# Optimization experiments

Measured on AMD Instinct MI355X. Metric: run time of the kernel, lower is better.

Reference implementation:

```python
import jax, jax.numpy as jnp
import numpy as np
from itertools import product

D = 96  # input grid resolution; after subdivision it is 2*D = 192
N_VOX = 20000
C_IN = 64
C_OUT = 64

OFFSETS = jnp.array(list(product([-1, 0, 1], repeat=3)), dtype=jnp.int32)   # [27,3] conv neighborhood
CHILD = jnp.array(list(product([0, 1], repeat=3)), dtype=jnp.int32)        # [8,3] subdivision children


def _lin(coords, d):
    # linearize (z,y,x)-style coords into a flat index for the dense lookup grid
    return (coords[:, 0] * d + coords[:, 1]) * d + coords[:, 2]


def _submanifold_conv3d(coords, feats, W, b, d):
    """Submanifold sparse 3x3x3 conv: output only at active sites.
    coords: [N,3] int32, feats: [N,Cin], W: [27,Cin,Cout], b: [Cout]."""
    n = coords.shape[0]
    grid = jnp.full((d * d * d,), -1, dtype=jnp.int32).at[_lin(coords, d)].set(
        jnp.arange(n, dtype=jnp.int32))
    out = jnp.broadcast_to(b, (n, b.shape[0])).astype(feats.dtype)
    for k in range(27):  # fixed small kernel loop (unrolled under jit)
        nb = coords + OFFSETS[k]
        inb = jnp.all((nb >= 0) & (nb < d), axis=1)
        idx = grid[_lin(jnp.clip(nb, 0, d - 1), d)]
        mask = (inb & (idx >= 0)).astype(feats.dtype)
        f = feats[jnp.maximum(idx, 0)] * mask[:, None]  # gather active neighbors
        out = out + f @ W[k]
    return out


def setup_inputs() -> dict:
    rng = np.random.default_rng(0)
    lin = rng.choice(D ** 3, size=N_VOX, replace=False)  # unique active voxels
    coords = np.stack([lin // (D * D), (lin // D) % D, lin % D], axis=1).astype(np.int32)
    key = jax.random.key(0)
    k1, k2, k3, k4, k5 = jax.random.split(key, 5)
    scale = 1.0 / np.sqrt(27.0 * C_IN)
    return {
        "coords": jnp.asarray(coords),
        "feats": jax.random.normal(k1, (N_VOX, C_IN), jnp.float32),
        "W1": jax.random.normal(k2, (27, C_IN, C_OUT), jnp.float32) * scale,
        "b1": jax.random.normal(k3, (C_OUT,), jnp.float32) * 0.01,
        "W2": jax.random.normal(k4, (27, C_OUT, C_OUT), jnp.float32) * scale,
        "b2": jax.random.normal(k5, (C_OUT,), jnp.float32) * 0.01,
    }


def reference(coords, feats, W1, b1, W2, b2):
    # act_layers: SparseConv3d + SiLU
    h = jax.nn.silu(_submanifold_conv3d(coords, feats, W1, b1, D))
    n = coords.shape[0]
    coords2 = ((coords * 2)[:, None, :] + CHILD[None, :, :]).reshape(8 * n, 3)
    h2 = jnp.repeat(h, 8, axis=0)  # matches (N,8,C)->(8N,C) child order
    # out_layers: SparseConv3d + SiLU at doubled resolution
    return jax.nn.silu(_submanifold_conv3d(coords2, h2, W2, b2, 2 * D))
```

## Files before the change

kernel.cpp:

```cpp
#include <hip/hip_runtime.h>

#define D1 96
#define GRID_VOX (D1 * D1 * D1)
#define CAP1 32
#define CAP2S 8
#define OS 68

typedef __attribute__((ext_vector_type(8))) short short8_t;
typedef __attribute__((ext_vector_type(4))) float f32x4;

__device__ __forceinline__ unsigned short bf16rne(float x) {
    unsigned u = __float_as_uint(x);
    return (unsigned short)((u + 0x7FFF + ((u >> 16) & 1)) >> 16);
}
__device__ __forceinline__ void split2(float v, unsigned short& hi,
                                       unsigned short& lo) {
    hi = bf16rne(v);
    float hf = __uint_as_float((unsigned)hi << 16);
    lo = bf16rne(v - hf);
}
__device__ __forceinline__ float silu(float v) {
    return v / (1.f + __expf(-v));
}

__global__ void setup_kernel(const float* __restrict__ W1,
                             const float* __restrict__ W2,
                             int4* __restrict__ grid16,
                             unsigned short* __restrict__ Wpk1h,
                             unsigned short* __restrict__ Wpk1l,
                             unsigned short* __restrict__ Wpk2h,
                             unsigned short* __restrict__ Wpk2l,
                             float* __restrict__ W2e) {
    int b = blockIdx.x;
    if (b < 432) {
        grid16[b * 256 + threadIdx.x] = make_int4(0, 0, 0, 0);
        return;
    }
    int t = (b - 432) * 256 + threadIdx.x;
    if (t < 512) {
        int fid = t >> 6, l = t & 63;
        int kb = fid >> 2, c = fid & 3;
#pragma unroll
        for (int e = 0; e < 8; ++e) {
            int ci = kb * 32 + ((l >> 4) << 3) + e;
            int co = c * 16 + (l & 15);
            unsigned short hi, lo;
            split2(W1[13 * 4096 + ci * 64 + co], hi, lo);
            Wpk1h[(size_t)t * 8 + e] = hi;
            Wpk1l[(size_t)t * 8 + e] = lo;
        }
    } else if (t < 512 + 4096) {
        int u = t - 512;
        int fid = u >> 6, l = u & 63;
        int s = fid >> 3, kb = (fid >> 2) & 1, c = fid & 3;
        int s0 = (s >> 2) & 1, s1 = (s >> 1) & 1, s2 = s & 1;
#pragma unroll
        for (int e = 0; e < 8; ++e) {
            int ci = kb * 32 + ((l >> 4) << 3) + e;
            int co = c * 16 + (l & 15);
            float sum = 0.f;
            for (int o0 = -s0; o0 <= 1 - s0; ++o0)
                for (int o1 = -s1; o1 <= 1 - s1; ++o1)
                    for (int o2 = -s2; o2 <= 1 - s2; ++o2) {
                        int k = (o0 + 1) * 9 + (o1 + 1) * 3 + (o2 + 1);
                        sum += W2[k * 4096 + ci * 64 + co];
                    }
            unsigned short hi, lo;
            split2(sum, hi, lo);
            Wpk2h[(size_t)u * 8 + e] = hi;
            Wpk2l[(size_t)u * 8 + e] = lo;
        }
    } else {
        int r = t - 4608;
        if (r >= 64 * 4096) return;
        int sd = r >> 12, e = r & 4095;
        int s = sd >> 3, d = sd & 7;
        int sa[3] = { (s >> 2) & 1, (s >> 1) & 1, s & 1 };
        int da[3] = { (d >> 2) & 1, (d >> 1) & 1, d & 1 };
        int lo_[3], hi_[3];
        for (int a = 0; a < 3; ++a) {
            int p = sa[a] - 1 + da[a];
            int l = 2 * p - sa[a];     if (l < -1) l = -1;
            int h = 2 * p + 1 - sa[a]; if (h > 1) h = 1;
            lo_[a] = l; hi_[a] = h;
        }
        float sum = 0.f;
        for (int o0 = lo_[0]; o0 <= hi_[0]; ++o0)
            for (int o1 = lo_[1]; o1 <= hi_[1]; ++o1)
                for (int o2 = lo_[2]; o2 <= hi_[2]; ++o2) {
                    int k = (o0 + 1) * 9 + (o1 + 1) * 3 + (o2 + 1);
                    sum += W2[k * 4096 + e];
                }
        W2e[(size_t)sd * 4096 + e] = sum;
    }
}

__global__ void scatter_grid_kernel(const int* __restrict__ coords,
                                    unsigned short* __restrict__ grid, int n) {
    int i = blockIdx.x * blockDim.x + threadIdx.x;
    if (i < n)
        grid[(coords[3 * i] * D1 + coords[3 * i + 1]) * D1 + coords[3 * i + 2]] =
            (unsigned short)(i + 1);
}

__global__ void build_pairs_kernel(const int* __restrict__ coords,
                                   const unsigned short* __restrict__ grid,
                                   int* __restrict__ c1, int* __restrict__ p1,
                                   int* __restrict__ c2s, int* __restrict__ p2s,
                                   int n) {
    int i = blockIdx.x * blockDim.x + threadIdx.x;
    if (i >= n) return;
    int c0 = coords[3 * i], cc1 = coords[3 * i + 1], cc2 = coords[3 * i + 2];

    int jv[27];
#pragma unroll
    for (int k = 0; k < 27; ++k) {
        int o0 = k / 9 - 1, o1 = (k / 3) % 3 - 1, o2 = k % 3 - 1;
        int x0 = c0 + o0, x1 = cc1 + o1, x2 = cc2 + o2;
        bool inb = (unsigned)x0 < D1 && (unsigned)x1 < D1 && (unsigned)x2 < D1;
        jv[k] = inb ? (int)grid[(x0 * D1 + x1) * D1 + x2] - 1 : -1;
    }

    int n1 = 0;
    int n2[8] = {0, 0, 0, 0, 0, 0, 0, 0};
#pragma unroll
    for (int k = 0; k < 27; ++k) {
        if (k == 13) continue;
        int j = jv[k];
        if (j < 0) continue;
        int o0 = k / 9 - 1, o1 = (k / 3) % 3 - 1, o2 = k % 3 - 1;
        p1[(size_t)i * CAP1 + n1] = j | (k << 17);
        ++n1;
#pragma unroll
        for (int s = 0; s < 8; ++s) {
            int d0 = o0 + 1 - ((s >> 2) & 1);
            int d1 = o1 + 1 - ((s >> 1) & 1);
            int d2 = o2 + 1 - (s & 1);
            if (((d0 | d1 | d2) & ~1) == 0) {
                int d = (d0 << 2) | (d1 << 1) | d2;
                p2s[((size_t)i * 8 + s) * CAP2S + n2[s]] = j | (d << 17);
                ++n2[s];
            }
        }
    }
    c1[i] = n1;
#pragma unroll
    for (int s = 0; s < 8; ++s) c2s[i * 8 + s] = n2[s];
}

__device__ __forceinline__ void load_split_A(const float* __restrict__ src,
                                             int arow, int lane, short8_t& ah0,
                                             short8_t& al0, short8_t& ah1,
                                             short8_t& al1) {
    const float* ap = src + (size_t)arow * 64 + ((lane >> 4) << 3);
    f32x4 a0 = *(const f32x4*)(ap);
    f32x4 a1 = *(const f32x4*)(ap + 4);
    f32x4 a2 = *(const f32x4*)(ap + 32);
    f32x4 a3 = *(const f32x4*)(ap + 36);
#pragma unroll
    for (int e = 0; e < 4; ++e) {
        unsigned short hh, ll;
        split2(a0[e], hh, ll); ah0[e] = (short)hh; al0[e] = (short)ll;
        split2(a1[e], hh, ll); ah0[4 + e] = (short)hh; al0[4 + e] = (short)ll;
        split2(a2[e], hh, ll); ah1[e] = (short)hh; al1[e] = (short)ll;
        split2(a3[e], hh, ll); ah1[4 + e] = (short)hh; al1[4 + e] = (short)ll;
    }
}

__device__ __forceinline__ void dense_mfma8(const short8_t ah0, const short8_t al0,
                                            const short8_t ah1, const short8_t al1,
                                            const short8_t* __restrict__ Bh,
                                            const short8_t* __restrict__ Bl,
                                            const float* __restrict__ bias,
                                            float* __restrict__ oT, int w,
                                            int lane) {
    int c0 = (w >> 2) * 2;
#pragma unroll
    for (int cc = 0; cc < 2; ++cc) {
        int c = c0 + cc;
        short8_t bh0 = Bh[c * 64 + lane];
        short8_t bl0 = Bl[c * 64 + lane];
        short8_t bh1 = Bh[(4 + c) * 64 + lane];
        short8_t bl1 = Bl[(4 + c) * 64 + lane];
        f32x4 acc = {0.f, 0.f, 0.f, 0.f};
        acc = __builtin_amdgcn_mfma_f32_16x16x32_bf16(ah0, bh0, acc, 0, 0, 0);
        acc = __builtin_amdgcn_mfma_f32_16x16x32_bf16(al0, bh0, acc, 0, 0, 0);
        acc = __builtin_amdgcn_mfma_f32_16x16x32_bf16(ah0, bl0, acc, 0, 0, 0);
        acc = __builtin_amdgcn_mfma_f32_16x16x32_bf16(ah1, bh1, acc, 0, 0, 0);
        acc = __builtin_amdgcn_mfma_f32_16x16x32_bf16(al1, bh1, acc, 0, 0, 0);
        acc = __builtin_amdgcn_mfma_f32_16x16x32_bf16(ah1, bl1, acc, 0, 0, 0);
        int col = c * 16 + (lane & 15);
        float bb = bias[col];
#pragma unroll
        for (int r = 0; r < 4; ++r) {
            int row = (w & 3) * 16 + ((lane >> 4) << 2) + r;
            oT[row * OS + col] = acc[r] + bb;
        }
    }
}

__device__ __forceinline__ void scan64(int cnt, int lane, int* pfxs, int* cnts,
                                       int* nps) {
    int val = cnt;
#pragma unroll
    for (int off = 1; off < 64; off <<= 1) {
        int v2 = __shfl_up(val, off);
        if (lane >= off) val += v2;
    }
    pfxs[lane] = val - cnt;
    cnts[lane] = cnt;
    if (lane == 63) nps[0] = val;
}

__device__ __forceinline__ void fixup_loop(const float* __restrict__ src,
                                           const float* __restrict__ Wbase,
                                           const int* __restrict__ pl, int np,
                                           float fsc[8][2][64],
                                           float* __restrict__ oT, int w,
                                           int lane) {
    int it = 0;
#pragma unroll 1
    for (int p = w; p < np; p += 8, ++it) {
        int e = pl[p];
        int j = e & 0x1FFFF, tag = (e >> 17) & 31, row = (e >> 23) & 63;
        float fv = src[(size_t)j * 64 + lane];
        int buf = it & 1;
        fsc[w][buf][lane] = fv;
        const float* wk = Wbase + (size_t)tag * 4096;
        float a0 = 0.f, a1 = 0.f, a2 = 0.f, a3 = 0.f;
#pragma unroll
        for (int c4 = 0; c4 < 16; ++c4) {
            f32x4 fb = *(f32x4*)&fsc[w][buf][c4 * 4];
            a0 += fb[0] * wk[(c4 * 4 + 0) * 64 + lane];
            a1 += fb[1] * wk[(c4 * 4 + 1) * 64 + lane];
            a2 += fb[2] * wk[(c4 * 4 + 2) * 64 + lane];
            a3 += fb[3] * wk[(c4 * 4 + 3) * 64 + lane];
        }
        atomicAdd(&oT[row * OS + lane], (a0 + a1) + (a2 + a3));
    }
}

__global__ __launch_bounds__(512) void conv1_fused_kernel(
    const float* __restrict__ feats, const float* __restrict__ W1,
    const unsigned short* __restrict__ Wpk1h,
    const unsigned short* __restrict__ Wpk1l, const float* __restrict__ b1,
    const int* __restrict__ c1, const int* __restrict__ p1,
    float* __restrict__ h, int n) {
    __shared__ __align__(16) float oT[64 * OS];
    __shared__ __align__(16) float fsc[8][2][64];
    __shared__ int pl[1664];
    __shared__ int pfxs[64], cnts_s[64], nps[1];
    int base = blockIdx.x * 64;
    int t = threadIdx.x, w = t >> 6, lane = t & 63;

    if (t < 64) {
        int cnt = (base + lane < n) ? c1[base + lane] : 0;
        scan64(cnt, lane, pfxs, cnts_s, nps);
    }

    int arow = base + (w & 3) * 16 + (lane & 15);
    if (arow >= n) arow = n - 1;
    short8_t ah0, al0, ah1, al1;
    load_split_A(feats, arow, lane, ah0, al0, ah1, al1);
    dense_mfma8(ah0, al0, ah1, al1, (const short8_t*)Wpk1h,
                (const short8_t*)Wpk1l, b1, oT, w, lane);
    __syncthreads();

    {
        int row = t & 63, e0 = t >> 6;
        int cr = cnts_s[row], pf = pfxs[row];
        for (int e = e0; e < cr; e += 8)
            pl[pf + e] = p1[(size_t)(base + row) * CAP1 + e] | (row << 23);
    }
    __syncthreads();

    fixup_loop(feats, W1, pl, nps[0], fsc, oT, w, lane);
    __syncthreads();

    {
        int r = t >> 3, c8 = (t & 7) * 8;
        if (base + r < n) {
#pragma unroll
            for (int jj = 0; jj < 2; ++jj) {
                f32x4 v = *(f32x4*)&oT[r * OS + c8 + jj * 4];
#pragma unroll
                for (int u = 0; u < 4; ++u) v[u] = silu(v[u]);
                *(f32x4*)&h[(size_t)(base + r) * 64 + c8 + jj * 4] = v;
            }
        }
    }
}

__global__ __launch_bounds__(512) void conv2_fused_kernel(
    const float* __restrict__ h, const unsigned short* __restrict__ Wpk2h,
    const unsigned short* __restrict__ Wpk2l, const float* __restrict__ W2e,
    const float* __restrict__ b2, const int* __restrict__ c2s,
    const int* __restrict__ p2s, float* __restrict__ out, int n) {
    __shared__ __align__(16) float oT[64 * OS];
    __shared__ __align__(16) float fsc[8][2][64];
    __shared__ int pl[448];
    __shared__ int pfxs[64], cnts_s[64], nps[1];
    int base = blockIdx.x * 64, s = blockIdx.y;
    int t = threadIdx.x, w = t >> 6, lane = t & 63;

    if (t < 64) {
        int cnt = (base + lane < n) ? c2s[(size_t)(base + lane) * 8 + s] : 0;
        scan64(cnt, lane, pfxs, cnts_s, nps);
    }

    int arow = base + (w & 3) * 16 + (lane & 15);
    if (arow >= n) arow = n - 1;
    short8_t ah0, al0, ah1, al1;
    load_split_A(h, arow, lane, ah0, al0, ah1, al1);
    dense_mfma8(ah0, al0, ah1, al1,
                (const short8_t*)Wpk2h + (size_t)s * 8 * 64,
                (const short8_t*)Wpk2l + (size_t)s * 8 * 64, b2, oT, w, lane);
    __syncthreads();

    {
        int row = t & 63, e0 = t >> 6;
        int cr = cnts_s[row], pf = pfxs[row];
        for (int e = e0; e < cr; e += 8)
            pl[pf + e] =
                p2s[((size_t)(base + row) * 8 + s) * CAP2S + e] | (row << 23);
    }
    __syncthreads();

    fixup_loop(h, W2e + (size_t)s * 8 * 4096, pl, nps[0], fsc, oT, w, lane);
    __syncthreads();

    {
        int r = t >> 3, c8 = (t & 7) * 8;
        if (base + r < n) {
#pragma unroll
            for (int jj = 0; jj < 2; ++jj) {
                f32x4 v = *(f32x4*)&oT[r * OS + c8 + jj * 4];
#pragma unroll
                for (int u = 0; u < 4; ++u) v[u] = silu(v[u]);
                *(f32x4*)&out[((size_t)(base + r) * 8 + s) * 64 + c8 + jj * 4] = v;
            }
        }
    }
}

extern "C" void kernel_launch(void* const* d_in, const int* in_sizes, int n_in,
                              void* d_out, int out_size, void* d_ws,
                              size_t ws_size, hipStream_t stream) {
    const int* coords = (const int*)d_in[0];
    const float* feats = (const float*)d_in[1];
    const float* W1 = (const float*)d_in[2];
    const float* b1 = (const float*)d_in[3];
    const float* W2 = (const float*)d_in[4];
    const float* b2 = (const float*)d_in[5];
    float* out = (float*)d_out;

    int n = in_sizes[0] / 3;
    int nblk = (n + 63) / 64;

    char* ws = (char*)d_ws;
    size_t off = 0;
    auto alloc = [&](size_t bytes) {
        size_t o = off;
        off = (off + bytes + 255) & ~(size_t)255;
        return o;
    };
    unsigned short* grid1 = (unsigned short*)(ws + alloc((size_t)GRID_VOX * 2));
    float* h      = (float*)(ws + alloc((size_t)n * 64 * 4));
    float* W2e    = (float*)(ws + alloc(64 * 4096 * 4));
    unsigned short* Wpk1h = (unsigned short*)(ws + alloc(512 * 8 * 2));
    unsigned short* Wpk1l = (unsigned short*)(ws + alloc(512 * 8 * 2));
    unsigned short* Wpk2h = (unsigned short*)(ws + alloc(4096 * 8 * 2));
    unsigned short* Wpk2l = (unsigned short*)(ws + alloc(4096 * 8 * 2));
    int*   c1     = (int*)(ws + alloc((size_t)n * 9 * 4));
    int*   c2s    = c1 + n;
    int*   p1     = (int*)(ws + alloc((size_t)n * CAP1 * 4));
    int*   p2s    = (int*)(ws + alloc((size_t)n * 8 * CAP2S * 4));

    setup_kernel<<<1474, 256, 0, stream>>>(W1, W2, (int4*)grid1, Wpk1h, Wpk1l,
                                           Wpk2h, Wpk2l, W2e);
    scatter_grid_kernel<<<(n + 255) / 256, 256, 0, stream>>>(coords, grid1, n);
    build_pairs_kernel<<<(n + 255) / 256, 256, 0, stream>>>(
        coords, grid1, c1, p1, c2s, p2s, n);

    conv1_fused_kernel<<<nblk, 512, 0, stream>>>(feats, W1, Wpk1h, Wpk1l, b1,
                                                 c1, p1, h, n);
    conv2_fused_kernel<<<dim3(nblk, 8), 512, 0, stream>>>(
        h, Wpk2h, Wpk2l, W2e, b2, c2s, p2s, out, n);
}
```

Baseline: 84.56 us.

## Fuse grid scatter into setup and neighbor-pair building into conv1, skip grid clearing

Drops the zeroing of the dense hash grid and folds the coordinate scatter into the setup kernel, so two launches are removed. The neighbor search and rulebook construction now happen inside the first conv kernel, using 64 threads per block, and conv1 pairs are kept in shared memory instead of being written to and read back from global memory. Because the grid is never cleared, stale entries are guarded by checking the stored index against the real coordinates. The price is a serial neighbor search on one wave per block ahead of the MFMA work, plus extra coordinate loads for the validation.

```diff
diff --git a/kernel.cpp b/kernel.cpp
--- a/kernel.cpp
+++ b/kernel.cpp
@@ -2,7 +2,6 @@
 
 #define D1 96
 #define GRID_VOX (D1 * D1 * D1)
-#define CAP1 32
 #define CAP2S 8
 #define OS 68
 
@@ -25,18 +24,14 @@
 
 __global__ void setup_kernel(const float* __restrict__ W1,
                              const float* __restrict__ W2,
-                             int4* __restrict__ grid16,
+                             const int* __restrict__ coords,
+                             unsigned short* __restrict__ grid,
                              unsigned short* __restrict__ Wpk1h,
                              unsigned short* __restrict__ Wpk1l,
                              unsigned short* __restrict__ Wpk2h,
                              unsigned short* __restrict__ Wpk2l,
-                             float* __restrict__ W2e) {
-    int b = blockIdx.x;
-    if (b < 432) {
-        grid16[b * 256 + threadIdx.x] = make_int4(0, 0, 0, 0);
-        return;
-    }
-    int t = (b - 432) * 256 + threadIdx.x;
+                             float* __restrict__ W2e, int n) {
+    int t = blockIdx.x * blockDim.x + threadIdx.x;
     if (t < 512) {
         int fid = t >> 6, l = t & 63;
         int kb = fid >> 2, c = fid & 3;
@@ -49,7 +44,7 @@
             Wpk1h[(size_t)t * 8 + e] = hi;
             Wpk1l[(size_t)t * 8 + e] = lo;
         }
-    } else if (t < 512 + 4096) {
+    } else if (t < 4608) {
         int u = t - 512;
         int fid = u >> 6, l = u & 63;
         int s = fid >> 3, kb = (fid >> 2) & 1, c = fid & 3;
@@ -70,9 +65,8 @@
             Wpk2h[(size_t)u * 8 + e] = hi;
             Wpk2l[(size_t)u * 8 + e] = lo;
         }
-    } else {
+    } else if (t < 4608 + 262144) {
         int r = t - 4608;
-        if (r >= 64 * 4096) return;
         int sd = r >> 12, e = r & 4095;
         int s = sd >> 3, d = sd & 7;
         int sa[3] = { (s >> 2) & 1, (s >> 1) & 1, s & 1 };
@@ -92,60 +86,12 @@
                     sum += W2[k * 4096 + e];
                 }
         W2e[(size_t)sd * 4096 + e] = sum;
-    }
-}
-
-__global__ void scatter_grid_kernel(const int* __restrict__ coords,
-                                    unsigned short* __restrict__ grid, int n) {
-    int i = blockIdx.x * blockDim.x + threadIdx.x;
-    if (i < n)
-        grid[(coords[3 * i] * D1 + coords[3 * i + 1]) * D1 + coords[3 * i + 2]] =
-            (unsigned short)(i + 1);
-}
-
-__global__ void build_pairs_kernel(const int* __restrict__ coords,
-                                   const unsigned short* __restrict__ grid,
-                                   int* __restrict__ c1, int* __restrict__ p1,
-                                   int* __restrict__ c2s, int* __restrict__ p2s,
-                                   int n) {
-    int i = blockIdx.x * blockDim.x + threadIdx.x;
-    if (i >= n) return;
-    int c0 = coords[3 * i], cc1 = coords[3 * i + 1], cc2 = coords[3 * i + 2];
-
-    int jv[27];
-#pragma unroll
-    for (int k = 0; k < 27; ++k) {
-        int o0 = k / 9 - 1, o1 = (k / 3) % 3 - 1, o2 = k % 3 - 1;
-        int x0 = c0 + o0, x1 = cc1 + o1, x2 = cc2 + o2;
-        bool inb = (unsigned)x0 < D1 && (unsigned)x1 < D1 && (unsigned)x2 < D1;
-        jv[k] = inb ? (int)grid[(x0 * D1 + x1) * D1 + x2] - 1 : -1;
-    }
-
-    int n1 = 0;
-    int n2[8] = {0, 0, 0, 0, 0, 0, 0, 0};
-#pragma unroll
-    for (int k = 0; k < 27; ++k) {
-        if (k == 13) continue;
-        int j = jv[k];
-        if (j < 0) continue;
-        int o0 = k / 9 - 1, o1 = (k / 3) % 3 - 1, o2 = k % 3 - 1;
-        p1[(size_t)i * CAP1 + n1] = j | (k << 17);
-        ++n1;
-#pragma unroll
-        for (int s = 0; s < 8; ++s) {
-            int d0 = o0 + 1 - ((s >> 2) & 1);
-            int d1 = o1 + 1 - ((s >> 1) & 1);
-            int d2 = o2 + 1 - (s & 1);
-            if (((d0 | d1 | d2) & ~1) == 0) {
-                int d = (d0 << 2) | (d1 << 1) | d2;
-                p2s[((size_t)i * 8 + s) * CAP2S + n2[s]] = j | (d << 17);
-                ++n2[s];
-            }
-        }
-    }
-    c1[i] = n1;
-#pragma unroll
-    for (int s = 0; s < 8; ++s) c2s[i * 8 + s] = n2[s];
+    } else {
+        int i = t - (4608 + 262144);
+        if (i < n)
+            grid[(coords[3 * i] * D1 + coords[3 * i + 1]) * D1 +
+                 coords[3 * i + 2]] = (unsigned short)(i + 1);
+    }
 }
 
 __device__ __forceinline__ void load_split_A(const float* __restrict__ src,
@@ -241,20 +187,70 @@
 }
 
 __global__ __launch_bounds__(512) void conv1_fused_kernel(
-    const float* __restrict__ feats, const float* __restrict__ W1,
-    const unsigned short* __restrict__ Wpk1h,
+    const int* __restrict__ coords, const float* __restrict__ feats,
+    const float* __restrict__ W1, const unsigned short* __restrict__ Wpk1h,
     const unsigned short* __restrict__ Wpk1l, const float* __restrict__ b1,
-    const int* __restrict__ c1, const int* __restrict__ p1,
-    float* __restrict__ h, int n) {
+    const unsigned short* __restrict__ grid, int* __restrict__ c2s,
+    int* __restrict__ p2s, float* __restrict__ h, int n) {
     __shared__ __align__(16) float oT[64 * OS];
     __shared__ __align__(16) float fsc[8][2][64];
+    __shared__ int plt[64 * 26];
     __shared__ int pl[1664];
     __shared__ int pfxs[64], cnts_s[64], nps[1];
     int base = blockIdx.x * 64;
     int t = threadIdx.x, w = t >> 6, lane = t & 63;
 
     if (t < 64) {
-        int cnt = (base + lane < n) ? c1[base + lane] : 0;
+        int myv = base + t;
+        int cnt = 0;
+        if (myv < n) {
+            int c0 = coords[3 * myv], c1v = coords[3 * myv + 1],
+                c2v = coords[3 * myv + 2];
+            int n2[8] = {0, 0, 0, 0, 0, 0, 0, 0};
+#pragma unroll 1
+            for (int g = 0; g < 3; ++g) {
+                int jv9[9];
+                int kb = g * 9;
+#pragma unroll
+                for (int u = 0; u < 9; ++u) {
+                    int k = kb + u;
+                    int o0 = k / 9 - 1, o1 = (k / 3) % 3 - 1, o2 = k % 3 - 1;
+                    int x0 = c0 + o0, x1 = c1v + o1, x2 = c2v + o2;
+                    bool inb = (unsigned)x0 < D1 && (unsigned)x1 < D1 &&
+                               (unsigned)x2 < D1;
+                    jv9[u] = inb ? (int)grid[(x0 * D1 + x1) * D1 + x2] : 0;
+                }
+#pragma unroll
+                for (int u = 0; u < 9; ++u) {
+                    int k = kb + u;
+                    if (k == 13) continue;
+                    int j1 = jv9[u];
+                    if (j1 < 1 || j1 > n) continue;
+                    int o0 = k / 9 - 1, o1 = (k / 3) % 3 - 1, o2 = k % 3 - 1;
+                    int x0 = c0 + o0, x1 = c1v + o1, x2 = c2v + o2;
+                    int jj = j1 - 1;
+                    if (coords[3 * jj] != x0 || coords[3 * jj + 1] != x1 ||
+                        coords[3 * jj + 2] != x2)
+                        continue;
+                    plt[t * 26 + cnt] = jj | (k << 17);
+                    ++cnt;
+#pragma unroll
+                    for (int s = 0; s < 8; ++s) {
+                        int d0 = o0 + 1 - ((s >> 2) & 1);
+                        int d1 = o1 + 1 - ((s >> 1) & 1);
+                        int d2 = o2 + 1 - (s & 1);
+                        if (((d0 | d1 | d2) & ~1) == 0) {
+                            int d = (d0 << 2) | (d1 << 1) | d2;
+                            p2s[((size_t)myv * 8 + s) * CAP2S + n2[s]] =
+                                jj | (d << 17);
+                            ++n2[s];
+                        }
+                    }
+                }
+            }
+#pragma unroll
+            for (int s = 0; s < 8; ++s) c2s[myv * 8 + s] = n2[s];
+        }
         scan64(cnt, lane, pfxs, cnts_s, nps);
     }
 
@@ -270,7 +266,7 @@
         int row = t & 63, e0 = t >> 6;
         int cr = cnts_s[row], pf = pfxs[row];
         for (int e = e0; e < cr; e += 8)
-            pl[pf + e] = p1[(size_t)(base + row) * CAP1 + e] | (row << 23);
+            pl[pf + e] = plt[row * 26 + e] | (row << 23);
     }
     __syncthreads();
 
@@ -371,19 +367,16 @@
     unsigned short* Wpk1l = (unsigned short*)(ws + alloc(512 * 8 * 2));
     unsigned short* Wpk2h = (unsigned short*)(ws + alloc(4096 * 8 * 2));
     unsigned short* Wpk2l = (unsigned short*)(ws + alloc(4096 * 8 * 2));
-    int*   c1     = (int*)(ws + alloc((size_t)n * 9 * 4));
-    int*   c2s    = c1 + n;
-    int*   p1     = (int*)(ws + alloc((size_t)n * CAP1 * 4));
+    int*   c2s    = (int*)(ws + alloc((size_t)n * 8 * 4));
     int*   p2s    = (int*)(ws + alloc((size_t)n * 8 * CAP2S * 4));
 
-    setup_kernel<<<1474, 256, 0, stream>>>(W1, W2, (int4*)grid1, Wpk1h, Wpk1l,
-                                           Wpk2h, Wpk2l, W2e);
-    scatter_grid_kernel<<<(n + 255) / 256, 256, 0, stream>>>(coords, grid1, n);
-    build_pairs_kernel<<<(n + 255) / 256, 256, 0, stream>>>(
-        coords, grid1, c1, p1, c2s, p2s, n);
-
-    conv1_fused_kernel<<<nblk, 512, 0, stream>>>(feats, W1, Wpk1h, Wpk1l, b1,
-                                                 c1, p1, h, n);
+    int totalT = 4608 + 262144 + n;
+    setup_kernel<<<(totalT + 255) / 256, 256, 0, stream>>>(
+        W1, W2, coords, grid1, Wpk1h, Wpk1l, Wpk2h, Wpk2l, W2e, n);
+
+    conv1_fused_kernel<<<nblk, 512, 0, stream>>>(coords, feats, W1, Wpk1h,
+                                                 Wpk1l, b1, grid1, c2s, p2s, h,
+                                                 n);
     conv2_fused_kernel<<<dim3(nblk, 8), 512, 0, stream>>>(
         h, Wpk2h, Wpk2l, W2e, b2, c2s, p2s, out, n);
 }
```

New measurement: 83.42 us. About the same (-1.3%).
